# Kernel optimization log

Measured on AMD Instinct MI355X. Metric: run time of the kernel, lower is better.

## Reference

```python
import jax, jax.numpy as jnp
import numpy as np

N, C, D = 8192, 16, 5

def setup_inputs() -> dict:
    key = jax.random.key(0)
    k1, k2 = jax.random.split(key)
    U = jax.random.normal(k1, (N, C), dtype=jnp.float32)
    ref = jax.random.normal(k2, (N, D), dtype=jnp.float32)
    return {"U": U, "ref": ref}

def reference(U, ref):
    # Exact Gaussian bilateral filter that the permutohedral lattice approximates:
    # out_i = sum_j exp(-0.5 * ||ref_i - ref_j||^2) * U_j  -  U_i
    sq = jnp.sum(ref * ref, axis=-1)                      # [N]
    # squared pairwise distances via gram trick: ||ri||^2 + ||rj||^2 - 2 ri.rj
    d2 = sq[:, None] + sq[None, :] - 2.0 * (ref @ ref.T)  # [N, N]
    W = jnp.exp(-0.5 * jnp.maximum(d2, 0.0))              # [N, N] Gaussian kernel
    return W @ U - U                                      # [N, C]
```

## Files before the change

kernel.cpp:

```cpp
#include <hip/hip_runtime.h>


#define N_ROWS 8192
#define C_CH   16
#define D_DIM  5
#define TPB    256
#define NSEG   32
#define NIB    (N_ROWS / TPB)
#define JPB    (N_ROWS / NSEG)

__global__ __launch_bounds__(TPB) void lg_pre(const float* __restrict__ ref,
                                              float* __restrict__ sqh) {
    const int j = blockIdx.x * TPB + threadIdx.x;
    float s = 0.0f;
#pragma unroll
    for (int d = 0; d < D_DIM; ++d) {
        const float v = ref[j * D_DIM + d];
        s = fmaf(v, v, s);
    }
    sqh[j] = -0.5f * s;
}

__global__ __launch_bounds__(TPB) void lg_main(const float* __restrict__ U,
                                               const float* __restrict__ ref,
                                               const float* __restrict__ sqh,
                                               float* __restrict__ part) {
    const int bid = blockIdx.x;
    const int ib  = bid % NIB;
    const int seg = bid / NIB;
    const int i   = ib * TPB + threadIdx.x;

    const float r0 = ref[i * D_DIM + 0];
    const float r1 = ref[i * D_DIM + 1];
    const float r2 = ref[i * D_DIM + 2];
    const float r3 = ref[i * D_DIM + 3];
    const float r4 = ref[i * D_DIM + 4];
    float ai = r0 * r0;
    ai = fmaf(r1, r1, ai);
    ai = fmaf(r2, r2, ai);
    ai = fmaf(r3, r3, ai);
    ai = fmaf(r4, r4, ai);
    ai = -0.5f * ai;

    float acc[C_CH];
#pragma unroll
    for (int c = 0; c < C_CH; ++c) acc[c] = 0.0f;

    const float4* __restrict__ U4 = reinterpret_cast<const float4*>(U);

    const int j0 = seg * JPB;
#pragma unroll 8
    for (int j = j0; j < j0 + JPB; ++j) {
        const float s0 = ref[j * D_DIM + 0];
        const float s1 = ref[j * D_DIM + 1];
        const float s2 = ref[j * D_DIM + 2];
        const float s3 = ref[j * D_DIM + 3];
        const float s4 = ref[j * D_DIM + 4];

        float e = ai + sqh[j];
        e = fmaf(r0, s0, e);
        e = fmaf(r1, s1, e);
        e = fmaf(r2, s2, e);
        e = fmaf(r3, s3, e);
        e = fmaf(r4, s4, e);
        const float w = __expf(e);

        const float4 u0 = U4[j * 4 + 0];
        const float4 u1 = U4[j * 4 + 1];
        const float4 u2 = U4[j * 4 + 2];
        const float4 u3 = U4[j * 4 + 3];

        acc[0]  = fmaf(w, u0.x, acc[0]);   acc[1]  = fmaf(w, u0.y, acc[1]);
        acc[2]  = fmaf(w, u0.z, acc[2]);   acc[3]  = fmaf(w, u0.w, acc[3]);
        acc[4]  = fmaf(w, u1.x, acc[4]);   acc[5]  = fmaf(w, u1.y, acc[5]);
        acc[6]  = fmaf(w, u1.z, acc[6]);   acc[7]  = fmaf(w, u1.w, acc[7]);
        acc[8]  = fmaf(w, u2.x, acc[8]);   acc[9]  = fmaf(w, u2.y, acc[9]);
        acc[10] = fmaf(w, u2.z, acc[10]);  acc[11] = fmaf(w, u2.w, acc[11]);
        acc[12] = fmaf(w, u3.x, acc[12]);  acc[13] = fmaf(w, u3.y, acc[13]);
        acc[14] = fmaf(w, u3.z, acc[14]);  acc[15] = fmaf(w, u3.w, acc[15]);
    }

    float4* p4 = reinterpret_cast<float4*>(part + ((size_t)seg * N_ROWS + i) * C_CH);
    p4[0] = make_float4(acc[0], acc[1], acc[2], acc[3]);
    p4[1] = make_float4(acc[4], acc[5], acc[6], acc[7]);
    p4[2] = make_float4(acc[8], acc[9], acc[10], acc[11]);
    p4[3] = make_float4(acc[12], acc[13], acc[14], acc[15]);
}

__global__ __launch_bounds__(TPB) void lg_reduce(const float* __restrict__ U,
                                                 const float* __restrict__ part,
                                                 float* __restrict__ out) {
    const int t = blockIdx.x * TPB + threadIdx.x;
    const float4 u = reinterpret_cast<const float4*>(U)[t];
    float4 s = make_float4(-u.x, -u.y, -u.z, -u.w);
    const float4* p = reinterpret_cast<const float4*>(part);
#pragma unroll
    for (int seg = 0; seg < NSEG; ++seg) {
        const float4 v = p[(size_t)seg * (N_ROWS * C_CH / 4) + t];
        s.x += v.x; s.y += v.y; s.z += v.z; s.w += v.w;
    }
    reinterpret_cast<float4*>(out)[t] = s;
}


__global__ __launch_bounds__(TPB) void lg_init(const float* __restrict__ U,
                                               float* __restrict__ out) {
    const int idx = blockIdx.x * TPB + threadIdx.x;
    if (idx < N_ROWS * C_CH) out[idx] = -U[idx];
}

__global__ __launch_bounds__(TPB) void lg_main_atomic(const float* __restrict__ U,
                                                      const float* __restrict__ ref,
                                                      float* __restrict__ out) {
    const int bid = blockIdx.x;
    const int ib  = bid % NIB;
    const int seg = bid / NIB;
    const int i   = ib * TPB + threadIdx.x;

    const float r0 = ref[i * D_DIM + 0];
    const float r1 = ref[i * D_DIM + 1];
    const float r2 = ref[i * D_DIM + 2];
    const float r3 = ref[i * D_DIM + 3];
    const float r4 = ref[i * D_DIM + 4];

    float acc[C_CH];
#pragma unroll
    for (int c = 0; c < C_CH; ++c) acc[c] = 0.0f;

    const float4* __restrict__ U4 = reinterpret_cast<const float4*>(U);
    const int j0 = seg * JPB;
#pragma unroll 4
    for (int j = j0; j < j0 + JPB; ++j) {
        const float d0 = r0 - ref[j * D_DIM + 0];
        const float d1 = r1 - ref[j * D_DIM + 1];
        const float d2 = r2 - ref[j * D_DIM + 2];
        const float d3 = r3 - ref[j * D_DIM + 3];
        const float d4 = r4 - ref[j * D_DIM + 4];
        float dsq = d0 * d0;
        dsq = fmaf(d1, d1, dsq); dsq = fmaf(d2, d2, dsq);
        dsq = fmaf(d3, d3, dsq); dsq = fmaf(d4, d4, dsq);
        const float w = __expf(-0.5f * dsq);

        const float4 u0 = U4[j * 4 + 0];
        const float4 u1 = U4[j * 4 + 1];
        const float4 u2 = U4[j * 4 + 2];
        const float4 u3 = U4[j * 4 + 3];
        acc[0]  = fmaf(w, u0.x, acc[0]);   acc[1]  = fmaf(w, u0.y, acc[1]);
        acc[2]  = fmaf(w, u0.z, acc[2]);   acc[3]  = fmaf(w, u0.w, acc[3]);
        acc[4]  = fmaf(w, u1.x, acc[4]);   acc[5]  = fmaf(w, u1.y, acc[5]);
        acc[6]  = fmaf(w, u1.z, acc[6]);   acc[7]  = fmaf(w, u1.w, acc[7]);
        acc[8]  = fmaf(w, u2.x, acc[8]);   acc[9]  = fmaf(w, u2.y, acc[9]);
        acc[10] = fmaf(w, u2.z, acc[10]);  acc[11] = fmaf(w, u2.w, acc[11]);
        acc[12] = fmaf(w, u3.x, acc[12]);  acc[13] = fmaf(w, u3.y, acc[13]);
        acc[14] = fmaf(w, u3.z, acc[14]);  acc[15] = fmaf(w, u3.w, acc[15]);
    }

    float* o = out + (size_t)i * C_CH;
#pragma unroll
    for (int c = 0; c < C_CH; ++c) atomicAdd(&o[c], acc[c]);
}

extern "C" void kernel_launch(void* const* d_in, const int* in_sizes, int n_in,
                              void* d_out, int out_size, void* d_ws, size_t ws_size,
                              hipStream_t stream) {
    const float* U   = (const float*)d_in[0];
    const float* ref = (const float*)d_in[1];
    float* out       = (float*)d_out;

    const size_t need = ((size_t)N_ROWS + (size_t)NSEG * N_ROWS * C_CH) * sizeof(float);
    if (ws_size >= need) {
        float* sqh  = (float*)d_ws;
        float* part = sqh + N_ROWS;
        hipLaunchKernelGGL(lg_pre, dim3(N_ROWS / TPB), dim3(TPB), 0, stream, ref, sqh);
        hipLaunchKernelGGL(lg_main, dim3(NIB * NSEG), dim3(TPB), 0, stream,
                           U, ref, sqh, part);
        hipLaunchKernelGGL(lg_reduce, dim3(N_ROWS * C_CH / 4 / TPB), dim3(TPB), 0,
                           stream, U, part, out);
    } else {
        hipLaunchKernelGGL(lg_init, dim3((N_ROWS * C_CH + TPB - 1) / TPB), dim3(TPB),
                           0, stream, U, out);
        hipLaunchKernelGGL(lg_main_atomic, dim3(NIB * NSEG), dim3(TPB), 0, stream,
                           U, ref, out);
    }
}
```

Measured before the change: 114.0 us.

## Pack log2e-scaled ref data, use exp2, and split j into more segments

Precomputes a 32-byte aligned per-point pack holding ref coordinates and the half squared norm, both pre-scaled by log2e, so the inner loop does one vector load and a native exp2 instead of five scalar loads, a separate norm load and expf. It also templates the segment count and uses 64 segments when workspace allows, doubling the grid for more parallelism. The cost is twice the partial-sum buffer traffic in the reduce kernel and a larger workspace requirement.

```diff
diff --git a/kernel.cpp b/kernel.cpp
--- a/kernel.cpp
+++ b/kernel.cpp
@@ -5,26 +5,45 @@
 #define C_CH   16
 #define D_DIM  5
 #define TPB    256
-#define NSEG   32
 #define NIB    (N_ROWS / TPB)
-#define JPB    (N_ROWS / NSEG)
+
+#if __has_builtin(__builtin_amdgcn_exp2f)
+#define EXP2(x) __builtin_amdgcn_exp2f(x)
+#else
+#define EXP2(x) exp2f(x)
+#endif
+
+#define LOG2E 1.4426950408889634f
+
+struct alignas(32) RefPack {
+    float s[8];
+};
 
 __global__ __launch_bounds__(TPB) void lg_pre(const float* __restrict__ ref,
-                                              float* __restrict__ sqh) {
+                                              RefPack* __restrict__ pack) {
     const int j = blockIdx.x * TPB + threadIdx.x;
-    float s = 0.0f;
-#pragma unroll
-    for (int d = 0; d < D_DIM; ++d) {
-        const float v = ref[j * D_DIM + d];
-        s = fmaf(v, v, s);
-    }
-    sqh[j] = -0.5f * s;
-}
-
+    float v0 = ref[j * D_DIM + 0];
+    float v1 = ref[j * D_DIM + 1];
+    float v2 = ref[j * D_DIM + 2];
+    float v3 = ref[j * D_DIM + 3];
+    float v4 = ref[j * D_DIM + 4];
+    float s = v0 * v0;
+    s = fmaf(v1, v1, s); s = fmaf(v2, v2, s);
+    s = fmaf(v3, v3, s); s = fmaf(v4, v4, s);
+    RefPack p;
+    p.s[0] = v0 * LOG2E; p.s[1] = v1 * LOG2E; p.s[2] = v2 * LOG2E;
+    p.s[3] = v3 * LOG2E; p.s[4] = v4 * LOG2E;
+    p.s[5] = -0.5f * LOG2E * s;
+    p.s[6] = 0.0f; p.s[7] = 0.0f;
+    pack[j] = p;
+}
+
+template <int NSEG>
 __global__ __launch_bounds__(TPB) void lg_main(const float* __restrict__ U,
                                                const float* __restrict__ ref,
-                                               const float* __restrict__ sqh,
+                                               const RefPack* __restrict__ pack,
                                                float* __restrict__ part) {
+    constexpr int JPB = N_ROWS / NSEG;
     const int bid = blockIdx.x;
     const int ib  = bid % NIB;
     const int seg = bid / NIB;
@@ -36,11 +55,9 @@
     const float r3 = ref[i * D_DIM + 3];
     const float r4 = ref[i * D_DIM + 4];
     float ai = r0 * r0;
-    ai = fmaf(r1, r1, ai);
-    ai = fmaf(r2, r2, ai);
-    ai = fmaf(r3, r3, ai);
-    ai = fmaf(r4, r4, ai);
-    ai = -0.5f * ai;
+    ai = fmaf(r1, r1, ai); ai = fmaf(r2, r2, ai);
+    ai = fmaf(r3, r3, ai); ai = fmaf(r4, r4, ai);
+    ai = -0.5f * LOG2E * ai;
 
     float acc[C_CH];
 #pragma unroll
@@ -49,21 +66,17 @@
     const float4* __restrict__ U4 = reinterpret_cast<const float4*>(U);
 
     const int j0 = seg * JPB;
-#pragma unroll 8
+#pragma unroll 4
     for (int j = j0; j < j0 + JPB; ++j) {
-        const float s0 = ref[j * D_DIM + 0];
-        const float s1 = ref[j * D_DIM + 1];
-        const float s2 = ref[j * D_DIM + 2];
-        const float s3 = ref[j * D_DIM + 3];
-        const float s4 = ref[j * D_DIM + 4];
-
-        float e = ai + sqh[j];
-        e = fmaf(r0, s0, e);
-        e = fmaf(r1, s1, e);
-        e = fmaf(r2, s2, e);
-        e = fmaf(r3, s3, e);
-        e = fmaf(r4, s4, e);
-        const float w = __expf(e);
+        const RefPack rp = pack[j];
+
+        float e = ai + rp.s[5];
+        e = fmaf(r0, rp.s[0], e);
+        e = fmaf(r1, rp.s[1], e);
+        e = fmaf(r2, rp.s[2], e);
+        e = fmaf(r3, rp.s[3], e);
+        e = fmaf(r4, rp.s[4], e);
+        const float w = EXP2(e);
 
         const float4 u0 = U4[j * 4 + 0];
         const float4 u1 = U4[j * 4 + 1];
@@ -87,6 +100,7 @@
     p4[3] = make_float4(acc[12], acc[13], acc[14], acc[15]);
 }
 
+template <int NSEG>
 __global__ __launch_bounds__(TPB) void lg_reduce(const float* __restrict__ U,
                                                  const float* __restrict__ part,
                                                  float* __restrict__ out) {
@@ -94,7 +108,7 @@
     const float4 u = reinterpret_cast<const float4*>(U)[t];
     float4 s = make_float4(-u.x, -u.y, -u.z, -u.w);
     const float4* p = reinterpret_cast<const float4*>(part);
-#pragma unroll
+#pragma unroll 8
     for (int seg = 0; seg < NSEG; ++seg) {
         const float4 v = p[(size_t)seg * (N_ROWS * C_CH / 4) + t];
         s.x += v.x; s.y += v.y; s.z += v.z; s.w += v.w;
@@ -112,6 +126,8 @@
 __global__ __launch_bounds__(TPB) void lg_main_atomic(const float* __restrict__ U,
                                                       const float* __restrict__ ref,
                                                       float* __restrict__ out) {
+    constexpr int NSEG = 32;
+    constexpr int JPB  = N_ROWS / NSEG;
     const int bid = blockIdx.x;
     const int ib  = bid % NIB;
     const int seg = bid / NIB;
@@ -167,19 +183,34 @@
     const float* ref = (const float*)d_in[1];
     float* out       = (float*)d_out;
 
-    const size_t need = ((size_t)N_ROWS + (size_t)NSEG * N_ROWS * C_CH) * sizeof(float);
-    if (ws_size >= need) {
-        float* sqh  = (float*)d_ws;
-        float* part = sqh + N_ROWS;
-        hipLaunchKernelGGL(lg_pre, dim3(N_ROWS / TPB), dim3(TPB), 0, stream, ref, sqh);
-        hipLaunchKernelGGL(lg_main, dim3(NIB * NSEG), dim3(TPB), 0, stream,
-                           U, ref, sqh, part);
-        hipLaunchKernelGGL(lg_reduce, dim3(N_ROWS * C_CH / 4 / TPB), dim3(TPB), 0,
-                           stream, U, part, out);
+    const size_t pack_bytes = (size_t)N_ROWS * sizeof(RefPack);
+    const size_t part_elems = [](int nseg) {
+        return (size_t)nseg * N_ROWS * C_CH;
+    }(1);
+
+    const size_t need64 = pack_bytes + 64 * part_elems * sizeof(float);
+    const size_t need32 = pack_bytes + 32 * part_elems * sizeof(float);
+
+    if (ws_size >= need64) {
+        RefPack* pack = (RefPack*)d_ws;
+        float* part   = (float*)((char*)d_ws + pack_bytes);
+        hipLaunchKernelGGL(lg_pre, dim3(N_ROWS / TPB), dim3(TPB), 0, stream, ref, pack);
+        hipLaunchKernelGGL((lg_main<64>), dim3(NIB * 64), dim3(TPB), 0, stream,
+                           U, ref, pack, part);
+        hipLaunchKernelGGL((lg_reduce<64>), dim3(N_ROWS * C_CH / 4 / TPB), dim3(TPB),
+                           0, stream, U, part, out);
+    } else if (ws_size >= need32) {
+        RefPack* pack = (RefPack*)d_ws;
+        float* part   = (float*)((char*)d_ws + pack_bytes);
+        hipLaunchKernelGGL(lg_pre, dim3(N_ROWS / TPB), dim3(TPB), 0, stream, ref, pack);
+        hipLaunchKernelGGL((lg_main<32>), dim3(NIB * 32), dim3(TPB), 0, stream,
+                           U, ref, pack, part);
+        hipLaunchKernelGGL((lg_reduce<32>), dim3(N_ROWS * C_CH / 4 / TPB), dim3(TPB),
+                           0, stream, U, part, out);
     } else {
         hipLaunchKernelGGL(lg_init, dim3((N_ROWS * C_CH + TPB - 1) / TPB), dim3(TPB),
                            0, stream, U, out);
-        hipLaunchKernelGGL(lg_main_atomic, dim3(NIB * NSEG), dim3(TPB), 0, stream,
+        hipLaunchKernelGGL(lg_main_atomic, dim3(NIB * 32), dim3(TPB), 0, stream,
                            U, ref, out);
     }
 }
```

Measured after the change: 119.3 us. +4.6%, slower.

## Compute Gaussian weights and weighted sum with split-bf16 MFMA tiles

Applied to the files above, without the earlier changes.

Replaces the scalar per-pair FMA loop with MFMA 16x16x32 bf16 instructions. The exponent (including the squared-norm terms folded in with log2e scaling) is produced by one MFMA using hi/lo bf16 splits of the coordinates, and the weighted accumulation over U uses three MFMAs (hi*hi, hi*lo, lo*hi) to approximate fp32 accuracy. A preprocessing kernel packs ref and U into permuted bf16 hi/lo layouts, the segment count drops to 16, and the partials are stored channel-major for the reduction. The aim is to move the dominant FMA work onto matrix cores and use exp2 directly, at the cost of extra packing work and split-precision error.

```diff
diff --git a/kernel.cpp b/kernel.cpp
--- a/kernel.cpp
+++ b/kernel.cpp
@@ -5,103 +5,204 @@
 #define C_CH   16
 #define D_DIM  5
 #define TPB    256
-#define NSEG   32
-#define NIB    (N_ROWS / TPB)
+#define NSEG   16
 #define JPB    (N_ROWS / NSEG)
-
-__global__ __launch_bounds__(TPB) void lg_pre(const float* __restrict__ ref,
-                                              float* __restrict__ sqh) {
-    const int j = blockIdx.x * TPB + threadIdx.x;
-    float s = 0.0f;
+#define NIB    128
+#define ONEBF  0x3F80u
+
+#if __has_builtin(__builtin_amdgcn_exp2f)
+#define EXP2(x) __builtin_amdgcn_exp2f(x)
+#else
+#define EXP2(x) exp2f(x)
+#endif
+
+#define LOG2E 1.4426950408889634f
+
+typedef __attribute__((ext_vector_type(8))) short bf16x8;
+typedef __attribute__((ext_vector_type(4))) float f32x4;
+
+__device__ __forceinline__ unsigned bhi(float x) {
+    return __float_as_uint(x) >> 16;
+}
+__device__ __forceinline__ float bhif(float x) {
+    return __uint_as_float(__float_as_uint(x) & 0xFFFF0000u);
+}
+
+__global__ __launch_bounds__(TPB) void lg_pre(const float* __restrict__ U,
+                                              const float* __restrict__ ref,
+                                              unsigned* __restrict__ refB,
+                                              unsigned* __restrict__ uph,
+                                              unsigned* __restrict__ upl) {
+    const int t = blockIdx.x * TPB + threadIdx.x;
+    if (t < N_ROWS) {
+        float b[D_DIM], r2 = 0.0f;
+#pragma unroll
+        for (int d = 0; d < D_DIM; ++d) {
+            const float r = ref[t * D_DIM + d];
+            b[d] = LOG2E * r;
+            r2 = fmaf(r, r, r2);
+        }
+        const float s2 = -0.5f * LOG2E * r2;
+        unsigned bh[D_DIM], bl[D_DIM];
+#pragma unroll
+        for (int d = 0; d < D_DIM; ++d) {
+            bh[d] = bhi(b[d]);
+            bl[d] = bhi(b[d] - bhif(b[d]));
+        }
+        const unsigned sh = bhi(s2);
+        const unsigned sl = bhi(s2 - bhif(s2));
+        unsigned o[16];
+        o[0] = bh[0] | (bh[1] << 16);  o[1] = bh[2] | (bh[3] << 16);
+        o[2] = bh[4] | (bl[0] << 16);  o[3] = bl[1] | (bl[2] << 16);
+        o[4] = bl[3] | (bl[4] << 16);  o[5] = bh[0] | (bh[1] << 16);
+        o[6] = bh[2] | (bh[3] << 16);  o[7] = bh[4];
+        o[8] = sh | (sl << 16);        o[9] = ONEBF | (ONEBF << 16);
+        o[10] = 0; o[11] = 0; o[12] = 0; o[13] = 0; o[14] = 0; o[15] = 0;
+        uint4* dst = reinterpret_cast<uint4*>(refB + (size_t)t * 16);
+        dst[0] = make_uint4(o[0], o[1], o[2], o[3]);
+        dst[1] = make_uint4(o[4], o[5], o[6], o[7]);
+        dst[2] = make_uint4(o[8], o[9], o[10], o[11]);
+        dst[3] = make_uint4(o[12], o[13], o[14], o[15]);
+    } else if (t < N_ROWS + (C_CH * N_ROWS / 2)) {
+        const int q = t - N_ROWS;
+        const int c = q >> 12;
+        const int p = q & 4095;
+        float u[2], lo[2];
+#pragma unroll
+        for (int h = 0; h < 2; ++h) {
+            const int idx = 2 * p + h;
+            const int blk = idx >> 5;
+            const int w32 = idx & 31;
+            const int G = w32 >> 3;
+            const int e = w32 & 7;
+            const int jm = blk * 32 + ((e < 4) ? (G * 4 + e)
+                                               : (16 + G * 4 + (e - 4)));
+            u[h] = U[(size_t)jm * C_CH + c];
+            lo[h] = u[h] - bhif(u[h]);
+        }
+        uph[(size_t)c * 4096 + p] = bhi(u[0]) | (bhi(u[1]) << 16);
+        upl[(size_t)c * 4096 + p] = bhi(lo[0]) | (bhi(lo[1]) << 16);
+    }
+}
+
+__global__ __launch_bounds__(TPB) void lg_mfma(const float* __restrict__ ref,
+                                               const unsigned* __restrict__ refB,
+                                               const unsigned* __restrict__ uph,
+                                               const unsigned* __restrict__ upl,
+                                               float* __restrict__ part) {
+    const int ib  = blockIdx.x & (NIB - 1);
+    const int seg = blockIdx.x / NIB;
+    const int tid = threadIdx.x;
+    const int wv  = tid >> 6;
+    const int l   = tid & 63;
+    const int li  = l & 15;
+    const int G   = l >> 4;
+    const int i   = ib * 64 + wv * 16 + li;
+
+    float a[D_DIM], r2 = 0.0f;
 #pragma unroll
     for (int d = 0; d < D_DIM; ++d) {
-        const float v = ref[j * D_DIM + d];
-        s = fmaf(v, v, s);
-    }
-    sqh[j] = -0.5f * s;
-}
-
-__global__ __launch_bounds__(TPB) void lg_main(const float* __restrict__ U,
-                                               const float* __restrict__ ref,
-                                               const float* __restrict__ sqh,
-                                               float* __restrict__ part) {
-    const int bid = blockIdx.x;
-    const int ib  = bid % NIB;
-    const int seg = bid / NIB;
-    const int i   = ib * TPB + threadIdx.x;
-
-    const float r0 = ref[i * D_DIM + 0];
-    const float r1 = ref[i * D_DIM + 1];
-    const float r2 = ref[i * D_DIM + 2];
-    const float r3 = ref[i * D_DIM + 3];
-    const float r4 = ref[i * D_DIM + 4];
-    float ai = r0 * r0;
-    ai = fmaf(r1, r1, ai);
-    ai = fmaf(r2, r2, ai);
-    ai = fmaf(r3, r3, ai);
-    ai = fmaf(r4, r4, ai);
-    ai = -0.5f * ai;
-
-    float acc[C_CH];
-#pragma unroll
-    for (int c = 0; c < C_CH; ++c) acc[c] = 0.0f;
-
-    const float4* __restrict__ U4 = reinterpret_cast<const float4*>(U);
+        a[d] = ref[i * D_DIM + d];
+        r2 = fmaf(a[d], a[d], r2);
+    }
+    const float a2 = -0.5f * LOG2E * r2;
+    unsigned ah[D_DIM], al[D_DIM];
+#pragma unroll
+    for (int d = 0; d < D_DIM; ++d) {
+        ah[d] = bhi(a[d]);
+        al[d] = bhi(a[d] - bhif(a[d]));
+    }
+    const unsigned a2h = bhi(a2);
+    const unsigned a2l = bhi(a2 - bhif(a2));
+
+    unsigned c0, c1, c2, c3;
+    if (G == 0) {
+        c0 = ah[0] | (ah[1] << 16); c1 = ah[2] | (ah[3] << 16);
+        c2 = ah[4] | (ah[0] << 16); c3 = ah[1] | (ah[2] << 16);
+    } else if (G == 1) {
+        c0 = ah[3] | (ah[4] << 16); c1 = al[0] | (al[1] << 16);
+        c2 = al[2] | (al[3] << 16); c3 = al[4];
+    } else if (G == 2) {
+        c0 = ONEBF | (ONEBF << 16); c1 = a2h | (a2l << 16);
+        c2 = 0; c3 = 0;
+    } else {
+        c0 = 0; c1 = 0; c2 = 0; c3 = 0;
+    }
+    const uint4 bfu = make_uint4(c0, c1, c2, c3);
+    const bf16x8 bfrag = __builtin_bit_cast(bf16x8, bfu);
+
+    f32x4 acc = {0.0f, 0.0f, 0.0f, 0.0f};
+    const f32x4 zero = {0.0f, 0.0f, 0.0f, 0.0f};
+
+    const uint4* RB = reinterpret_cast<const uint4*>(refB);
+    const uint4* UH = reinterpret_cast<const uint4*>(uph);
+    const uint4* UL = reinterpret_cast<const uint4*>(upl);
 
     const int j0 = seg * JPB;
-#pragma unroll 8
-    for (int j = j0; j < j0 + JPB; ++j) {
-        const float s0 = ref[j * D_DIM + 0];
-        const float s1 = ref[j * D_DIM + 1];
-        const float s2 = ref[j * D_DIM + 2];
-        const float s3 = ref[j * D_DIM + 3];
-        const float s4 = ref[j * D_DIM + 4];
-
-        float e = ai + sqh[j];
-        e = fmaf(r0, s0, e);
-        e = fmaf(r1, s1, e);
-        e = fmaf(r2, s2, e);
-        e = fmaf(r3, s3, e);
-        e = fmaf(r4, s4, e);
-        const float w = __expf(e);
-
-        const float4 u0 = U4[j * 4 + 0];
-        const float4 u1 = U4[j * 4 + 1];
-        const float4 u2 = U4[j * 4 + 2];
-        const float4 u3 = U4[j * 4 + 3];
-
-        acc[0]  = fmaf(w, u0.x, acc[0]);   acc[1]  = fmaf(w, u0.y, acc[1]);
-        acc[2]  = fmaf(w, u0.z, acc[2]);   acc[3]  = fmaf(w, u0.w, acc[3]);
-        acc[4]  = fmaf(w, u1.x, acc[4]);   acc[5]  = fmaf(w, u1.y, acc[5]);
-        acc[6]  = fmaf(w, u1.z, acc[6]);   acc[7]  = fmaf(w, u1.w, acc[7]);
-        acc[8]  = fmaf(w, u2.x, acc[8]);   acc[9]  = fmaf(w, u2.y, acc[9]);
-        acc[10] = fmaf(w, u2.z, acc[10]);  acc[11] = fmaf(w, u2.w, acc[11]);
-        acc[12] = fmaf(w, u3.x, acc[12]);  acc[13] = fmaf(w, u3.y, acc[13]);
-        acc[14] = fmaf(w, u3.z, acc[14]);  acc[15] = fmaf(w, u3.w, acc[15]);
-    }
-
-    float4* p4 = reinterpret_cast<float4*>(part + ((size_t)seg * N_ROWS + i) * C_CH);
-    p4[0] = make_float4(acc[0], acc[1], acc[2], acc[3]);
-    p4[1] = make_float4(acc[4], acc[5], acc[6], acc[7]);
-    p4[2] = make_float4(acc[8], acc[9], acc[10], acc[11]);
-    p4[3] = make_float4(acc[12], acc[13], acc[14], acc[15]);
+#pragma unroll 2
+    for (int js = 0; js < JPB / 32; ++js) {
+        const int jb = j0 + js * 32;
+
+        const uint4 rb1 = RB[(size_t)(jb + li) * 4 + G];
+        const uint4 rb2 = RB[(size_t)(jb + 16 + li) * 4 + G];
+
+        const f32x4 e1 = __builtin_amdgcn_mfma_f32_16x16x32_bf16(
+            __builtin_bit_cast(bf16x8, rb1), bfrag, zero, 0, 0, 0);
+        const f32x4 e2 = __builtin_amdgcn_mfma_f32_16x16x32_bf16(
+            __builtin_bit_cast(bf16x8, rb2), bfrag, zero, 0, 0, 0);
+
+        const float w0 = EXP2(e1[0]);
+        const float w1 = EXP2(e1[1]);
+        const float w2 = EXP2(e1[2]);
+        const float w3 = EXP2(e1[3]);
+        const float w4 = EXP2(e2[0]);
+        const float w5 = EXP2(e2[1]);
+        const float w6 = EXP2(e2[2]);
+        const float w7 = EXP2(e2[3]);
+
+        const unsigned h0 = (__float_as_uint(w1) & 0xFFFF0000u) | (__float_as_uint(w0) >> 16);
+        const unsigned h1 = (__float_as_uint(w3) & 0xFFFF0000u) | (__float_as_uint(w2) >> 16);
+        const unsigned h2 = (__float_as_uint(w5) & 0xFFFF0000u) | (__float_as_uint(w4) >> 16);
+        const unsigned h3 = (__float_as_uint(w7) & 0xFFFF0000u) | (__float_as_uint(w6) >> 16);
+        const float q0 = w0 - bhif(w0), q1 = w1 - bhif(w1);
+        const float q2 = w2 - bhif(w2), q3 = w3 - bhif(w3);
+        const float q4 = w4 - bhif(w4), q5 = w5 - bhif(w5);
+        const float q6 = w6 - bhif(w6), q7 = w7 - bhif(w7);
+        const unsigned g0 = (__float_as_uint(q1) & 0xFFFF0000u) | (__float_as_uint(q0) >> 16);
+        const unsigned g1 = (__float_as_uint(q3) & 0xFFFF0000u) | (__float_as_uint(q2) >> 16);
+        const unsigned g2 = (__float_as_uint(q5) & 0xFFFF0000u) | (__float_as_uint(q4) >> 16);
+        const unsigned g3 = (__float_as_uint(q7) & 0xFFFF0000u) | (__float_as_uint(q6) >> 16);
+
+        const bf16x8 wh = __builtin_bit_cast(bf16x8, make_uint4(h0, h1, h2, h3));
+        const bf16x8 wl = __builtin_bit_cast(bf16x8, make_uint4(g0, g1, g2, g3));
+
+        const size_t uidx = (size_t)li * 1024 + (jb >> 3) + G;
+        const bf16x8 uh = __builtin_bit_cast(bf16x8, UH[uidx]);
+        const bf16x8 ul = __builtin_bit_cast(bf16x8, UL[uidx]);
+
+        acc = __builtin_amdgcn_mfma_f32_16x16x32_bf16(uh, wh, acc, 0, 0, 0);
+        acc = __builtin_amdgcn_mfma_f32_16x16x32_bf16(uh, wl, acc, 0, 0, 0);
+        acc = __builtin_amdgcn_mfma_f32_16x16x32_bf16(ul, wh, acc, 0, 0, 0);
+    }
+
+#pragma unroll
+    for (int q = 0; q < 4; ++q) {
+        part[(size_t)(seg * C_CH + G * 4 + q) * N_ROWS + i] = acc[q];
+    }
 }
 
 __global__ __launch_bounds__(TPB) void lg_reduce(const float* __restrict__ U,
                                                  const float* __restrict__ part,
                                                  float* __restrict__ out) {
     const int t = blockIdx.x * TPB + threadIdx.x;
-    const float4 u = reinterpret_cast<const float4*>(U)[t];
-    float4 s = make_float4(-u.x, -u.y, -u.z, -u.w);
-    const float4* p = reinterpret_cast<const float4*>(part);
-#pragma unroll
-    for (int seg = 0; seg < NSEG; ++seg) {
-        const float4 v = p[(size_t)seg * (N_ROWS * C_CH / 4) + t];
-        s.x += v.x; s.y += v.y; s.z += v.z; s.w += v.w;
-    }
-    reinterpret_cast<float4*>(out)[t] = s;
-}
-
+    const int i = t & (N_ROWS - 1);
+    const int c = t >> 13;
+    float s = 0.0f;
+#pragma unroll 4
+    for (int seg = 0; seg < NSEG; ++seg)
+        s += part[(size_t)(seg * C_CH + c) * N_ROWS + i];
+    out[(size_t)i * C_CH + c] = s - U[(size_t)i * C_CH + c];
+}
 
 __global__ __launch_bounds__(TPB) void lg_init(const float* __restrict__ U,
                                                float* __restrict__ out) {
@@ -112,25 +213,19 @@
 __global__ __launch_bounds__(TPB) void lg_main_atomic(const float* __restrict__ U,
                                                       const float* __restrict__ ref,
                                                       float* __restrict__ out) {
-    const int bid = blockIdx.x;
-    const int ib  = bid % NIB;
-    const int seg = bid / NIB;
-    const int i   = ib * TPB + threadIdx.x;
-
-    const float r0 = ref[i * D_DIM + 0];
-    const float r1 = ref[i * D_DIM + 1];
-    const float r2 = ref[i * D_DIM + 2];
-    const float r3 = ref[i * D_DIM + 3];
+    constexpr int NS = 32, JP = N_ROWS / NS, NI = N_ROWS / TPB;
+    const int ib = blockIdx.x % NI, sg = blockIdx.x / NI;
+    const int i = ib * TPB + threadIdx.x;
+    const float r0 = ref[i * D_DIM + 0], r1 = ref[i * D_DIM + 1];
+    const float r2 = ref[i * D_DIM + 2], r3 = ref[i * D_DIM + 3];
     const float r4 = ref[i * D_DIM + 4];
-
     float acc[C_CH];
 #pragma unroll
     for (int c = 0; c < C_CH; ++c) acc[c] = 0.0f;
-
     const float4* __restrict__ U4 = reinterpret_cast<const float4*>(U);
-    const int j0 = seg * JPB;
+    const int j0 = sg * JP;
 #pragma unroll 4
-    for (int j = j0; j < j0 + JPB; ++j) {
+    for (int j = j0; j < j0 + JP; ++j) {
         const float d0 = r0 - ref[j * D_DIM + 0];
         const float d1 = r1 - ref[j * D_DIM + 1];
         const float d2 = r2 - ref[j * D_DIM + 2];
@@ -140,11 +235,8 @@
         dsq = fmaf(d1, d1, dsq); dsq = fmaf(d2, d2, dsq);
         dsq = fmaf(d3, d3, dsq); dsq = fmaf(d4, d4, dsq);
         const float w = __expf(-0.5f * dsq);
-
-        const float4 u0 = U4[j * 4 + 0];
-        const float4 u1 = U4[j * 4 + 1];
-        const float4 u2 = U4[j * 4 + 2];
-        const float4 u3 = U4[j * 4 + 3];
+        const float4 u0 = U4[j * 4 + 0], u1 = U4[j * 4 + 1];
+        const float4 u2 = U4[j * 4 + 2], u3 = U4[j * 4 + 3];
         acc[0]  = fmaf(w, u0.x, acc[0]);   acc[1]  = fmaf(w, u0.y, acc[1]);
         acc[2]  = fmaf(w, u0.z, acc[2]);   acc[3]  = fmaf(w, u0.w, acc[3]);
         acc[4]  = fmaf(w, u1.x, acc[4]);   acc[5]  = fmaf(w, u1.y, acc[5]);
@@ -154,7 +246,6 @@
         acc[12] = fmaf(w, u3.x, acc[12]);  acc[13] = fmaf(w, u3.y, acc[13]);
         acc[14] = fmaf(w, u3.z, acc[14]);  acc[15] = fmaf(w, u3.w, acc[15]);
     }
-
     float* o = out + (size_t)i * C_CH;
 #pragma unroll
     for (int c = 0; c < C_CH; ++c) atomicAdd(&o[c], acc[c]);
@@ -167,19 +258,28 @@
     const float* ref = (const float*)d_in[1];
     float* out       = (float*)d_out;
 
-    const size_t need = ((size_t)N_ROWS + (size_t)NSEG * N_ROWS * C_CH) * sizeof(float);
+    const size_t refB_b = (size_t)N_ROWS * 64;
+    const size_t upk_b  = (size_t)C_CH * N_ROWS * 2;
+    const size_t part_b = (size_t)NSEG * C_CH * N_ROWS * 4;
+    const size_t need   = refB_b + 2 * upk_b + part_b;
+
     if (ws_size >= need) {
-        float* sqh  = (float*)d_ws;
-        float* part = sqh + N_ROWS;
-        hipLaunchKernelGGL(lg_pre, dim3(N_ROWS / TPB), dim3(TPB), 0, stream, ref, sqh);
-        hipLaunchKernelGGL(lg_main, dim3(NIB * NSEG), dim3(TPB), 0, stream,
-                           U, ref, sqh, part);
-        hipLaunchKernelGGL(lg_reduce, dim3(N_ROWS * C_CH / 4 / TPB), dim3(TPB), 0,
-                           stream, U, part, out);
+        unsigned* refB = (unsigned*)d_ws;
+        unsigned* uph  = (unsigned*)((char*)d_ws + refB_b);
+        unsigned* upl  = (unsigned*)((char*)d_ws + refB_b + upk_b);
+        float* part    = (float*)((char*)d_ws + refB_b + 2 * upk_b);
+
+        const int pre_threads = N_ROWS + C_CH * N_ROWS / 2;
+        hipLaunchKernelGGL(lg_pre, dim3(pre_threads / TPB), dim3(TPB), 0, stream,
+                           U, ref, refB, uph, upl);
+        hipLaunchKernelGGL(lg_mfma, dim3(NIB * NSEG), dim3(TPB), 0, stream,
+                           ref, refB, uph, upl, part);
+        hipLaunchKernelGGL(lg_reduce, dim3(N_ROWS * C_CH / TPB), dim3(TPB),
+                           0, stream, U, part, out);
     } else {
         hipLaunchKernelGGL(lg_init, dim3((N_ROWS * C_CH + TPB - 1) / TPB), dim3(TPB),
                            0, stream, U, out);
-        hipLaunchKernelGGL(lg_main_atomic, dim3(NIB * NSEG), dim3(TPB), 0, stream,
-                           U, ref, out);
-    }
-}
+        hipLaunchKernelGGL(lg_main_atomic, dim3((N_ROWS / TPB) * 32), dim3(TPB),
+                           0, stream, U, ref, out);
+    }
+}
```

After: 107.9 us. 1.06x faster.
